# Performance work log

Measured on AMD Instinct MI355X. Metric: run time of the kernel, lower is better.

The kernel has to match this reference:

```python
import jax, jax.numpy as jnp
import numpy as np

HEADS = 16
DIM_HEAD = 64
SCALE = DIM_HEAD ** -0.5


def setup_inputs() -> dict:
    key = jax.random.key(0)
    ks = jax.random.split(key, 7)
    B, Nq, Dq = 16, 4096, 1024
    Nc, Dc = 77, 768
    inner = HEADS * DIM_HEAD  # 1024
    return {
        "x": jax.random.normal(ks[0], (B, Nq, Dq), jnp.float32),
        "context": jax.random.normal(ks[1], (B, Nc, Dc), jnp.float32),
        "Wq": jax.random.normal(ks[2], (Dq, inner), jnp.float32) * (Dq ** -0.5),
        "Wk": jax.random.normal(ks[3], (Dc, inner), jnp.float32) * (Dc ** -0.5),
        "Wv": jax.random.normal(ks[4], (Dc, inner), jnp.float32) * (Dc ** -0.5),
        "Wo": jax.random.normal(ks[5], (inner, Dq), jnp.float32) * (inner ** -0.5),
        "bo": jnp.zeros((Dq,), jnp.float32),
    }


def reference(x, context, Wq, Wk, Wv, Wo, bo):
    B, Nq, _ = x.shape
    Nc = context.shape[1]
    # projections (no bias), split heads: [B, H, N, Dh]
    q = (x @ Wq).reshape(B, Nq, HEADS, DIM_HEAD).transpose(0, 2, 1, 3)
    k = (context @ Wk).reshape(B, Nc, HEADS, DIM_HEAD).transpose(0, 2, 1, 3)
    v = (context @ Wv).reshape(B, Nc, HEADS, DIM_HEAD).transpose(0, 2, 1, 3)
    sim = jnp.einsum('bhid,bhjd->bhij', q, k) * SCALE
    attn = jax.nn.softmax(sim, axis=-1)
    out = jnp.einsum('bhij,bhjd->bhid', attn, v)
    out = out.transpose(0, 2, 1, 3).reshape(B, Nq, HEADS * DIM_HEAD)
    # to_out linear (dropout is identity at eval)
    return out @ Wo + bo
```

## Files before the change

### kernel.cpp

```cpp
#include <hip/hip_runtime.h>

typedef unsigned short u16;
typedef __bf16 bf16x8 __attribute__((ext_vector_type(8)));
typedef unsigned short u16x8 __attribute__((ext_vector_type(8)));
typedef float f32x4 __attribute__((ext_vector_type(4)));

namespace {
constexpr int kB = 16;
constexpr int kHeads = 16, kDh = 64;
constexpr int kNcPadS = 80;
constexpr int kNcPadV = 96;

constexpr size_t oWqT = 0;
constexpr size_t oWoT = oWqT + (size_t)1024 * 1024 * 2;
constexpr size_t oWkT = oWoT + (size_t)1024 * 1024 * 2;
constexpr size_t oWvT = oWkT + (size_t)1024 * 768 * 2;
constexpr size_t oCtx = oWvT + (size_t)1024 * 768 * 2;
constexpr size_t oKp  = oCtx + (size_t)1232 * 768 * 2;
constexpr size_t oVp  = oKp + (size_t)kB * kHeads * kNcPadS * kDh * 2;
constexpr size_t oQ   = oVp + (size_t)kB * kHeads * kDh * kNcPadV * 2;
}

__device__ __forceinline__ u16 f2b(float f) {
    __bf16 h = (__bf16)f;
    return __builtin_bit_cast(u16, h);
}
__device__ __forceinline__ bf16x8 ldfrag(const u16* p) {
    return __builtin_bit_cast(bf16x8, *reinterpret_cast<const u16x8*>(p));
}
__device__ __forceinline__ f32x4 mfma16(bf16x8 a, bf16x8 b, f32x4 c) {
    return __builtin_amdgcn_mfma_f32_16x16x32_bf16(a, b, c, 0, 0, 0);
}
__device__ __forceinline__ void gload16(const u16* g, u16* lds) {
    __builtin_amdgcn_global_load_lds(
        (const __attribute__((address_space(1))) void*)g,
        (__attribute__((address_space(3))) void*)lds, 16, 0, 0);
}

#define VMCNT(N) asm volatile("s_waitcnt vmcnt(" #N ")" ::: "memory")
#define LGKM0    asm volatile("s_waitcnt lgkmcnt(0)" ::: "memory")
#define BARRIER  do { __builtin_amdgcn_s_barrier(); asm volatile("" ::: "memory"); } while (0)

__device__ __forceinline__ void stage_u(const u16* gp, u16* unit, int tid, int kt) {
#pragma unroll
    for (int i = 0; i < 2; ++i) {
        int g = tid + i * 512;
        int prs = g >> 3;
        int s0 = (g & 7) ^ (prs & 7);
        gload16(gp + (size_t)(prs * 2 + (s0 >> 2)) * 1024 + kt + (s0 & 3) * 8,
                unit + ((g >> 6) << 9));
    }
}

__global__ __launch_bounds__(256) void xconv_kernel(const float* __restrict__ x, u16* __restrict__ xb) {
    size_t i = (size_t)blockIdx.x * 256 + threadIdx.x;
    const float4* s = reinterpret_cast<const float4*>(x) + 2 * i;
    float4 v0 = s[0], v1 = s[1];
    u16x8 pk = { f2b(v0.x), f2b(v0.y), f2b(v0.z), f2b(v0.w),
                 f2b(v1.x), f2b(v1.y), f2b(v1.z), f2b(v1.w) };
    *reinterpret_cast<u16x8*>(xb + 8 * i) = pk;
}

__global__ __launch_bounds__(256) void prep2_kernel(
    const float* __restrict__ Wq, const float* __restrict__ Wk,
    const float* __restrict__ Wv, const float* __restrict__ Wo,
    const float* __restrict__ ctx, u16* __restrict__ ws) {
    __shared__ u16 tl[64][72];
    int b = blockIdx.x;
    int tid = threadIdx.x;
    if (b < 896) {
        const float* S; u16* D; int t, DC;
        if (b < 256)       { S = Wq; D = ws + oWqT / 2; t = b;       DC = 1024; }
        else if (b < 512)  { S = Wo; D = ws + oWoT / 2; t = b - 256; DC = 1024; }
        else if (b < 704)  { S = Wk; D = ws + oWkT / 2; t = b - 512; DC = 768;  }
        else               { S = Wv; D = ws + oWvT / 2; t = b - 704; DC = 768;  }
        int tk = t >> 4, tn = t & 15;
        int k0 = tk * 64, n0 = tn * 64;
#pragma unroll
        for (int i = 0; i < 4; ++i) {
            int r = (tid >> 4) + i * 16;
            float4 v = *reinterpret_cast<const float4*>(S + (size_t)(k0 + r) * 1024 + n0 + (tid & 15) * 4);
            u16 e0 = f2b(v.x), e1 = f2b(v.y), e2 = f2b(v.z), e3 = f2b(v.w);
            u16* p = &tl[r][(tid & 15) * 4];
            p[0] = e0; p[1] = e1; p[2] = e2; p[3] = e3;
        }
        __syncthreads();
#pragma unroll
        for (int i = 0; i < 2; ++i) {
            int n = (tid >> 3) + i * 32;
            u16x8 o;
#pragma unroll
            for (int j = 0; j < 8; ++j) o[j] = tl[(tid & 7) * 8 + j][n];
            *reinterpret_cast<u16x8*>(D + (size_t)(n0 + n) * DC + k0 + (tid & 7) * 8) = o;
        }
        return;
    }
    if (b < 896 + 462) {
        size_t i = (size_t)(b - 896) * 2048 + tid * 8;
        const float4* s = reinterpret_cast<const float4*>(ctx) + i / 4;
        float4 v0 = s[0], v1 = s[1];
        u16x8 pk = { f2b(v0.x), f2b(v0.y), f2b(v0.z), f2b(v0.w),
                     f2b(v1.x), f2b(v1.y), f2b(v1.z), f2b(v1.w) };
        *reinterpret_cast<u16x8*>(ws + oCtx / 2 + i) = pk;
        return;
    }
    size_t j = (size_t)(b - 896 - 462) * 2048 + tid * 8;
    u16x8 z = {0, 0, 0, 0, 0, 0, 0, 0};
    *reinterpret_cast<u16x8*>(ws + oKp / 2 + j) = z;
}

__global__ __launch_bounds__(64) void kv_kernel(u16* __restrict__ ws) {
    const u16* ctxb = ws + oCtx / 2;
    const u16* WkT = ws + oWkT / 2;
    const u16* WvT = ws + oWvT / 2;
    u16* Kp = ws + oKp / 2;
    u16* Vp = ws + oVp / 2;
    int l = threadIdx.x;
    int mt = blockIdx.x >> 6;
    int nt = blockIdx.x & 63;
    int rowA = mt * 16 + (l & 15);
    int rowB = nt * 16 + (l & 15);
    int koff = (l >> 4) * 8;
    f32x4 accK = {0.f, 0.f, 0.f, 0.f}, accV = {0.f, 0.f, 0.f, 0.f};
    for (int k = 0; k < 768; k += 32) {
        bf16x8 a  = ldfrag(ctxb + rowA * 768 + k + koff);
        bf16x8 bk = ldfrag(WkT + rowB * 768 + k + koff);
        bf16x8 bv = ldfrag(WvT + rowB * 768 + k + koff);
        accK = mfma16(a, bk, accK);
        accV = mfma16(a, bv, accV);
    }
    int c = nt * 16 + (l & 15);
    int h = c >> 6, d = c & 63;
#pragma unroll
    for (int r = 0; r < 4; ++r) {
        int row = mt * 16 + (l >> 4) * 4 + r;
        int b = row / 77, j = row - b * 77;
        Kp[((size_t)(b * 16 + h) * kNcPadS + j) * kDh + d] = f2b(accK[r] * 0.125f);
        Vp[((size_t)(b * 16 + h) * kDh + d) * kNcPadV + j] = f2b(accV[r]);
    }
}

#define GPHASE(RLO, KS, READB, STAGE, VM) do {                                  \
    if (READB) { _Pragma("unroll") for (int c = 0; c < 4; ++c)                  \
        fb[c] = ldfrag(bU##KS + (wn * 4 + c) * 512 + rdoff); }                  \
    _Pragma("unroll") for (int r = 0; r < 4; ++r)                               \
        fa[r] = ldfrag(aU##KS + (wm * 8 + (RLO) + r) * 512 + rdoff);            \
    STAGE;                                                                      \
    BARRIER; LGKM0;                                                             \
    __builtin_amdgcn_sched_barrier(0);                                          \
    __builtin_amdgcn_s_setprio(1);                                              \
    _Pragma("unroll") for (int r = 0; r < 4; ++r)                               \
        _Pragma("unroll") for (int c = 0; c < 4; ++c)                           \
            acc[(RLO) + r][c] = mfma16(fa[r], fb[c], acc[(RLO) + r][c]);        \
    __builtin_amdgcn_s_setprio(0);                                              \
    VM;                                                                         \
    BARRIER;                                                                    \
} while (0)

#define GEMM_LOOP(aGp, bGp)                                                                          \
    stage_u(aGp, &sm[0][0][0][0], tid, 0);                                                           \
    stage_u(bGp, &sm[1][0][0][0], tid, 0);                                                           \
    stage_u(aGp, &sm[0][0][1][0], tid, 32);                                                          \
    stage_u(bGp, &sm[1][0][1][0], tid, 32);                                                          \
    stage_u(aGp, &sm[0][1][0][0], tid, 64);                                                          \
    stage_u(bGp, &sm[1][1][0][0], tid, 64);                                                          \
    VMCNT(8); BARRIER;                                                                               \
    for (int t = 0; t < 16; ++t) {                                                                   \
        const int d = t & 1, e = d ^ 1;                                                              \
        const u16* aU0 = &sm[0][d][0][0];                                                            \
        const u16* aU1 = &sm[0][d][1][0];                                                            \
        const u16* bU0 = &sm[1][d][0][0];                                                            \
        const u16* bU1 = &sm[1][d][1][0];                                                            \
        bf16x8 fa[4], fb[4];                                                                         \
        GPHASE(0, 0, true,  { if (t < 15) stage_u(aGp, &sm[0][e][1][0], tid, (t + 1) * 64 + 32); },  \
               {});                                                                                  \
        GPHASE(4, 0, false, { if (t < 15) stage_u(bGp, &sm[1][e][1][0], tid, (t + 1) * 64 + 32); },  \
               { if (t < 15) { VMCNT(8); } else { VMCNT(0); } });                                    \
        GPHASE(0, 1, true,  { if (t < 14) stage_u(aGp, &sm[0][d][0][0], tid, (t + 2) * 64); },       \
               {});                                                                                  \
        GPHASE(4, 1, false, { if (t < 14) stage_u(bGp, &sm[1][d][0][0], tid, (t + 2) * 64); },       \
               { if (t < 14) { VMCNT(8); } else if (t == 14) { VMCNT(4); } });                       \
    }

__global__ __launch_bounds__(512) void qproj_kernel(const u16* __restrict__ xb, u16* __restrict__ ws) {
    __shared__ u16 sm[2][2][2][8192];
    const u16* WqT = ws + oWqT / 2;
    u16* qb = ws + oQ / 2;
    int tid = threadIdx.x;
    int lane = tid & 63;
    int w = tid >> 6, wm = w >> 2, wn = w & 3;
    int lr = lane & 15, lr2 = lr >> 1;
    const int rdoff = lr2 * 64 + (((((lane & 1) << 2) | (lane >> 4))) ^ lr2) * 8;
    int bid = blockIdx.x;
    int wg = (bid & 7) * 128 + (bid >> 3);
    int bm = wg >> 2, bn = wg & 3;

    const u16* aG = xb + (size_t)(bm * 256) * 1024;
    const u16* bG = WqT + (size_t)(bn * 256) * 1024;

    f32x4 acc[8][4] = {};
    GEMM_LOOP(aG, bG);

#pragma unroll
    for (int r = 0; r < 8; ++r)
#pragma unroll
        for (int c = 0; c < 4; ++c)
#pragma unroll
            for (int reg = 0; reg < 4; ++reg) {
                int row = bm * 256 + wm * 128 + r * 16 + (lane >> 4) * 4 + reg;
                int col = bn * 256 + wn * 64 + c * 16 + lr;
                qb[(size_t)row * 1024 + col] = f2b(acc[r][c][reg]);
            }
}

__global__ __launch_bounds__(256) void attn_kernel(u16* __restrict__ ws) {
    u16* qb = ws + oQ / 2;
    const u16* Kp = ws + oKp / 2;
    const u16* Vp = ws + oVp / 2;
    __shared__ u16 P[4][16][128];
    int tid = threadIdx.x;
    int w = tid >> 6, lane = tid & 63;
    int bt = blockIdx.x >> 4;
    int h = blockIdx.x & 15;
    int b = bt >> 6;
    int rowbase = bt * 64 + w * 16;

    for (int ii = tid; ii < 128; ii += 256) {
        int wv = ii >> 5, rem = ii & 31;
        int rr = rem >> 1, uu = 10 + (rem & 1);
        u16x8 z = {0, 0, 0, 0, 0, 0, 0, 0};
        *reinterpret_cast<u16x8*>(&P[wv][rr][(uu ^ (rr & 7)) * 8]) = z;
    }

    const u16* Kh = Kp + (size_t)(b * 16 + h) * kNcPadS * kDh;
    const u16* Vh = Vp + (size_t)(b * 16 + h) * kDh * kNcPadV;

    int c = lane & 15;
    int g8 = (lane >> 4) * 8;

    u16x8 bmask[3];
#pragma unroll
    for (int kti = 0; kti < 3; ++kti)
#pragma unroll
        for (int j = 0; j < 8; ++j)
            bmask[kti][j] = (kti * 32 + g8 + j < 77) ? (u16)0x3F80 : (u16)0;

    f32x4 s[5] = {};
#pragma unroll
    for (int ks = 0; ks < 64; ks += 32) {
        bf16x8 a = ldfrag(qb + (size_t)(rowbase + c) * 1024 + h * 64 + ks + g8);
#pragma unroll
        for (int nt = 0; nt < 5; ++nt) {
            bf16x8 bb = ldfrag(Kh + (nt * 16 + c) * kDh + ks + g8);
            s[nt] = mfma16(a, bb, s[nt]);
        }
    }
#pragma unroll
    for (int nt = 0; nt < 5; ++nt)
#pragma unroll
        for (int r = 0; r < 4; ++r) {
            int row = (lane >> 4) * 4 + r;
            P[w][row][(((nt * 2) + (c >> 3)) ^ (row & 7)) * 8 + (c & 7)] = f2b(__expf(s[nt][r]));
        }
    __syncthreads();
    f32x4 o[4] = {};
    f32x4 msum = {0.f, 0.f, 0.f, 0.f};
#pragma unroll
    for (int kti = 0; kti < 3; ++kti) {
        int kt = kti * 32;
        bf16x8 a = ldfrag(&P[w][c][((((kt + g8) >> 3)) ^ (c & 7)) * 8]);
#pragma unroll
        for (int nt = 0; nt < 4; ++nt) {
            bf16x8 bb = ldfrag(Vh + (nt * 16 + c) * kNcPadV + kt + g8);
            o[nt] = mfma16(a, bb, o[nt]);
        }
        msum = mfma16(a, __builtin_bit_cast(bf16x8, bmask[kti]), msum);
    }
#pragma unroll
    for (int r = 0; r < 4; ++r) {
        float rinv = 1.f / msum[r];
#pragma unroll
        for (int nt = 0; nt < 4; ++nt) {
            int row = rowbase + (lane >> 4) * 4 + r;
            qb[(size_t)row * 1024 + h * 64 + nt * 16 + c] = f2b(o[nt][r] * rinv);
        }
    }
}

__global__ __launch_bounds__(512) void outproj_kernel(u16* __restrict__ ws, const float* __restrict__ bo,
                                                      float* __restrict__ out) {
    __shared__ u16 sm[2][2][2][8192];
    const u16* qb = ws + oQ / 2;
    const u16* WoT = ws + oWoT / 2;
    int tid = threadIdx.x;
    int lane = tid & 63;
    int w = tid >> 6, wm = w >> 2, wn = w & 3;
    int lr = lane & 15, lr2 = lr >> 1;
    const int rdoff = lr2 * 64 + (((((lane & 1) << 2) | (lane >> 4))) ^ lr2) * 8;
    int bid = blockIdx.x;
    int wg = (bid & 7) * 128 + (bid >> 3);
    int bm = wg >> 2, bn = wg & 3;

    const u16* aG = qb + (size_t)(bm * 256) * 1024;
    const u16* bG = WoT + (size_t)(bn * 256) * 1024;

    f32x4 acc[8][4] = {};
    GEMM_LOOP(aG, bG);

#pragma unroll
    for (int c = 0; c < 4; ++c) {
        int col = bn * 256 + wn * 64 + c * 16 + lr;
        float bias = bo[col];
#pragma unroll
        for (int r = 0; r < 8; ++r)
#pragma unroll
            for (int reg = 0; reg < 4; ++reg) {
                int row = bm * 256 + wm * 128 + r * 16 + (lane >> 4) * 4 + reg;
                out[(size_t)row * 1024 + col] = acc[r][c][reg] + bias;
            }
    }
}

extern "C" void kernel_launch(void* const* d_in, const int* in_sizes, int n_in,
                              void* d_out, int out_size, void* d_ws, size_t ws_size,
                              hipStream_t stream) {
    const float* x   = (const float*)d_in[0];
    const float* ctx = (const float*)d_in[1];
    const float* Wq  = (const float*)d_in[2];
    const float* Wk  = (const float*)d_in[3];
    const float* Wv  = (const float*)d_in[4];
    const float* Wo  = (const float*)d_in[5];
    const float* bo  = (const float*)d_in[6];
    float* out = (float*)d_out;
    u16* ws = (u16*)d_ws;
    u16* xb = (u16*)d_out;
    (void)in_sizes; (void)n_in; (void)out_size; (void)ws_size;

    xconv_kernel<<<32768, 256, 0, stream>>>(x, xb);
    prep2_kernel<<<896 + 462 + 1408, 256, 0, stream>>>(Wq, Wk, Wv, Wo, ctx, ws);
    kv_kernel<<<77 * 64, 64, 0, stream>>>(ws);
    qproj_kernel<<<1024, 512, 0, stream>>>(xb, ws);
    attn_kernel<<<1024 * 16, 256, 0, stream>>>(ws);
    outproj_kernel<<<1024, 512, 0, stream>>>(ws, bo, out);
}
```

Before: 584.5 us.

## Fuse attention into Q-projection GEMM epilogue via LDS-staged Q tiles

The Q projection kernel now writes its accumulator tile into shared memory in MFMA fragment layout, then each wave (owning one head's 64 columns and 128 rows) runs the cross-attention softmax and PV product directly, with K/V fragments held in registers. This removes the separate attention kernel launch and the round-trip of the Q tensor through global memory. In exchange it adds extra LDS (an 8x1536 P buffer) and register pressure in the GEMM kernel, which may lower occupancy. The attention part runs serially per wave after the GEMM.

```diff
diff --git a/kernel.cpp b/kernel.cpp
--- a/kernel.cpp
+++ b/kernel.cpp
@@ -50,6 +50,9 @@
         gload16(gp + (size_t)(prs * 2 + (s0 >> 2)) * 1024 + kt + (s0 & 3) * 8,
                 unit + ((g >> 6) << 9));
     }
+}
+__device__ __forceinline__ int pp16(int row16, int k32) {
+    return (row16 >> 1) * 64 + (((((row16 & 1) << 2) | (k32 >> 3)) ^ ((row16 >> 1) & 7)) * 8) + (k32 & 7);
 }
 
 __global__ __launch_bounds__(256) void xconv_kernel(const float* __restrict__ x, u16* __restrict__ xb) {
@@ -182,8 +185,9 @@
                { if (t < 14) { VMCNT(8); } else if (t == 14) { VMCNT(4); } });                       \
     }
 
-__global__ __launch_bounds__(512) void qproj_kernel(const u16* __restrict__ xb, u16* __restrict__ ws) {
+__global__ __launch_bounds__(512) void qproj_attn_kernel(const u16* __restrict__ xb, u16* __restrict__ ws) {
     __shared__ u16 sm[2][2][2][8192];
+    __shared__ u16 Pb[8][1536];
     const u16* WqT = ws + oWqT / 2;
     u16* qb = ws + oQ / 2;
     int tid = threadIdx.x;
@@ -201,88 +205,85 @@
     f32x4 acc[8][4] = {};
     GEMM_LOOP(aG, bG);
 
+    u16* smf = &sm[0][0][0][0];
+    u16* qw = smf + (size_t)w * 8192;
+    u16* Pw = &Pb[w][0];
+    int g = lane >> 4, g8 = g * 8;
+
 #pragma unroll
     for (int r = 0; r < 8; ++r)
 #pragma unroll
-        for (int c = 0; c < 4; ++c)
-#pragma unroll
-            for (int reg = 0; reg < 4; ++reg) {
-                int row = bm * 256 + wm * 128 + r * 16 + (lane >> 4) * 4 + reg;
-                int col = bn * 256 + wn * 64 + c * 16 + lr;
-                qb[(size_t)row * 1024 + col] = f2b(acc[r][c][reg]);
-            }
-}
-
-__global__ __launch_bounds__(256) void attn_kernel(u16* __restrict__ ws) {
-    u16* qb = ws + oQ / 2;
-    const u16* Kp = ws + oKp / 2;
-    const u16* Vp = ws + oVp / 2;
-    __shared__ u16 P[4][16][128];
-    int tid = threadIdx.x;
-    int w = tid >> 6, lane = tid & 63;
-    int bt = blockIdx.x >> 4;
-    int h = blockIdx.x & 15;
-    int b = bt >> 6;
-    int rowbase = bt * 64 + w * 16;
-
-    for (int ii = tid; ii < 128; ii += 256) {
-        int wv = ii >> 5, rem = ii & 31;
-        int rr = rem >> 1, uu = 10 + (rem & 1);
+        for (int c = 0; c < 4; ++c) {
+            int d = c * 16 + lr;
+            int unit = r * 2 + (d >> 5);
+            int k32 = d & 31;
+#pragma unroll
+            for (int reg = 0; reg < 4; ++reg)
+                qw[unit * 512 + pp16(g * 4 + reg, k32)] = f2b(acc[r][c][reg]);
+        }
+    {
         u16x8 z = {0, 0, 0, 0, 0, 0, 0, 0};
-        *reinterpret_cast<u16x8*>(&P[wv][rr][(uu ^ (rr & 7)) * 8]) = z;
-    }
-
-    const u16* Kh = Kp + (size_t)(b * 16 + h) * kNcPadS * kDh;
-    const u16* Vh = Vp + (size_t)(b * 16 + h) * kDh * kNcPadV;
-
-    int c = lane & 15;
-    int g8 = (lane >> 4) * 8;
-
+        *reinterpret_cast<u16x8*>(Pw + 2 * 512 + lane * 8) = z;
+    }
+    int b = bm >> 4;
+    int h = bn * 4 + wn;
+    const u16* Kh = ws + oKp / 2 + (size_t)(b * 16 + h) * kNcPadS * kDh;
+    const u16* Vh = ws + oVp / 2 + (size_t)(b * 16 + h) * kDh * kNcPadV;
+    bf16x8 kf[5][2], vf[3][4];
+#pragma unroll
+    for (int nt = 0; nt < 5; ++nt)
+#pragma unroll
+        for (int kc = 0; kc < 2; ++kc)
+            kf[nt][kc] = ldfrag(Kh + (nt * 16 + lr) * 64 + kc * 32 + g8);
+#pragma unroll
+    for (int kti = 0; kti < 3; ++kti)
+#pragma unroll
+        for (int nt = 0; nt < 4; ++nt)
+            vf[kti][nt] = ldfrag(Vh + (nt * 16 + lr) * kNcPadV + kti * 32 + g8);
     u16x8 bmask[3];
 #pragma unroll
     for (int kti = 0; kti < 3; ++kti)
 #pragma unroll
         for (int j = 0; j < 8; ++j)
             bmask[kti][j] = (kti * 32 + g8 + j < 77) ? (u16)0x3F80 : (u16)0;
-
-    f32x4 s[5] = {};
-#pragma unroll
-    for (int ks = 0; ks < 64; ks += 32) {
-        bf16x8 a = ldfrag(qb + (size_t)(rowbase + c) * 1024 + h * 64 + ks + g8);
-#pragma unroll
-        for (int nt = 0; nt < 5; ++nt) {
-            bf16x8 bb = ldfrag(Kh + (nt * 16 + c) * kDh + ks + g8);
-            s[nt] = mfma16(a, bb, s[nt]);
-        }
-    }
-#pragma unroll
-    for (int nt = 0; nt < 5; ++nt)
-#pragma unroll
-        for (int r = 0; r < 4; ++r) {
-            int row = (lane >> 4) * 4 + r;
-            P[w][row][(((nt * 2) + (c >> 3)) ^ (row & 7)) * 8 + (c & 7)] = f2b(__expf(s[nt][r]));
-        }
-    __syncthreads();
-    f32x4 o[4] = {};
-    f32x4 msum = {0.f, 0.f, 0.f, 0.f};
-#pragma unroll
-    for (int kti = 0; kti < 3; ++kti) {
-        int kt = kti * 32;
-        bf16x8 a = ldfrag(&P[w][c][((((kt + g8) >> 3)) ^ (c & 7)) * 8]);
-#pragma unroll
-        for (int nt = 0; nt < 4; ++nt) {
-            bf16x8 bb = ldfrag(Vh + (nt * 16 + c) * kNcPadV + kt + g8);
-            o[nt] = mfma16(a, bb, o[nt]);
-        }
-        msum = mfma16(a, __builtin_bit_cast(bf16x8, bmask[kti]), msum);
-    }
-#pragma unroll
-    for (int r = 0; r < 4; ++r) {
-        float rinv = 1.f / msum[r];
-#pragma unroll
-        for (int nt = 0; nt < 4; ++nt) {
-            int row = rowbase + (lane >> 4) * 4 + r;
-            qb[(size_t)row * 1024 + h * 64 + nt * 16 + c] = f2b(o[nt][r] * rinv);
+    LGKM0;
+    __builtin_amdgcn_sched_barrier(0);
+
+#pragma unroll 1
+    for (int rb = 0; rb < 8; ++rb) {
+        f32x4 s[5] = {};
+#pragma unroll
+        for (int kc = 0; kc < 2; ++kc) {
+            bf16x8 a = ldfrag(qw + (rb * 2 + kc) * 512 + rdoff);
+#pragma unroll
+            for (int nt = 0; nt < 5; ++nt) s[nt] = mfma16(a, kf[nt][kc], s[nt]);
+        }
+#pragma unroll
+        for (int nt = 0; nt < 5; ++nt)
+#pragma unroll
+            for (int reg = 0; reg < 4; ++reg) {
+                int j = nt * 16 + lr;
+                Pw[(j >> 5) * 512 + pp16(g * 4 + reg, j & 31)] = f2b(__expf(s[nt][reg]));
+            }
+        LGKM0;
+        __builtin_amdgcn_sched_barrier(0);
+        f32x4 o[4] = {};
+        f32x4 msum = {0.f, 0.f, 0.f, 0.f};
+#pragma unroll
+        for (int kti = 0; kti < 3; ++kti) {
+            bf16x8 a = ldfrag(Pw + kti * 512 + rdoff);
+#pragma unroll
+            for (int nt = 0; nt < 4; ++nt) o[nt] = mfma16(a, vf[kti][nt], o[nt]);
+            msum = mfma16(a, __builtin_bit_cast(bf16x8, bmask[kti]), msum);
+        }
+        LGKM0;
+#pragma unroll
+        for (int reg = 0; reg < 4; ++reg) {
+            float rinv = 1.f / msum[reg];
+            int row = bm * 256 + wm * 128 + rb * 16 + g * 4 + reg;
+#pragma unroll
+            for (int nt = 0; nt < 4; ++nt)
+                qb[(size_t)row * 1024 + h * 64 + nt * 16 + lr] = f2b(o[nt][reg] * rinv);
         }
     }
 }
@@ -339,7 +340,6 @@
     xconv_kernel<<<32768, 256, 0, stream>>>(x, xb);
     prep2_kernel<<<896 + 462 + 1408, 256, 0, stream>>>(Wq, Wk, Wv, Wo, ctx, ws);
     kv_kernel<<<77 * 64, 64, 0, stream>>>(ws);
-    qproj_kernel<<<1024, 512, 0, stream>>>(xb, ws);
-    attn_kernel<<<1024 * 16, 256, 0, stream>>>(ws);
+    qproj_attn_kernel<<<1024, 512, 0, stream>>>(xb, ws);
     outproj_kernel<<<1024, 512, 0, stream>>>(ws, bo, out);
 }
```

Result: faster. 503.1 us (-13.9%).
